# Kernel optimization log

Measured on AMD Instinct MI355X. Metric: run time of the kernel, lower is better.

Reference implementation:

```python
import jax, jax.numpy as jnp
import numpy as np

B = 1048576  # batch size
EPS_CLAMP_LO = 1e-6
EPS_CLAMP_HI = 1.0 - 1e-6


def _build_mask():
    # mask[k, i, j] = 1 iff i + j == k, flattened to [19, 100]
    i = np.arange(10)
    m = np.zeros((19, 10, 10), dtype=np.float32)
    ii, jj = np.meshgrid(i, i, indexing='ij')
    m[(ii + jj).ravel(), ii.ravel(), jj.ravel()] = 1.0
    return jnp.asarray(m.reshape(19, 100))


def setup_inputs() -> dict:
    key = jax.random.key(0)
    k1, k2, k3, k4 = jax.random.split(key, 4)
    # concept probabilities: uniform then normalize rows to sum 1
    p1 = jax.random.uniform(k1, (B, 10), dtype=jnp.float32)
    p1 = p1 / p1.sum(axis=1, keepdims=True)
    p2 = jax.random.uniform(k2, (B, 10), dtype=jnp.float32)
    p2 = p2 / p2.sum(axis=1, keepdims=True)
    # learnable permutation-tree weights (binaryTreeLogicNet leaf maps)
    W1 = jax.random.uniform(k3, (10, 10), dtype=jnp.float32)
    W2 = jax.random.uniform(k4, (10, 10), dtype=jnp.float32)
    mask = _build_mask()
    return {"p1": p1, "p2": p2, "W1": W1, "W2": W2, "mask": mask}


def _minmax_norm(W):
    lo = W.min(axis=1, keepdims=True)
    hi = W.max(axis=1, keepdims=True)
    return (W - lo) / (hi - lo + 1e-8)


def reference(p1, p2, W1, W2, mask):
    # input_to_leaf: learned soft permutation with minmax-normalized weights
    p1p = p1 @ _minmax_norm(W1)                      # [B,10]
    p2p = p2 @ _minmax_norm(W2)                      # [B,10]
    # MinMaxAggregator graded AND at andness=1.0 -> elementwise min over all pairs
    s = jnp.minimum(p1p[:, :, None], p2p[:, None, :])  # [B,10,10]
    one_minus = 1.0 - jnp.clip(s, EPS_CLAMP_LO, EPS_CLAMP_HI)
    log_one_minus = jnp.log(one_minus + 1e-12).reshape(-1, 100)  # [B,100]
    # fused masked reduction over all 19 sum bins: [B,100] @ [100,19]
    log_prod = log_one_minus @ mask.T                # [B,19]
    y_prob = 1.0 - jnp.exp(log_prod)                 # smooth OR per sum class
    y_prob = y_prob / (y_prob.sum(axis=1, keepdims=True) + 1e-9)
    return y_prob
```

## Files before the change

kernel.cpp:

```cpp
#include <hip/hip_runtime.h>


#define NBLOCKS 4096

__global__ __launch_bounds__(256) void bacon_main(
    const float* __restrict__ p1, const float* __restrict__ p2,
    const float* __restrict__ W1, const float* __restrict__ W2,
    float* __restrict__ out)
{
    __shared__ __align__(16) float s_out[4864];
    __shared__ __align__(16) float s_w[240];

    const int t = threadIdx.x;
    const int blk = blockIdx.x;

    float a[10], b[10];
    {
        const float2* g1 = (const float2*)p1 + (size_t)blk * 1280 + t * 5;
        const float2* g2 = (const float2*)p2 + (size_t)blk * 1280 + t * 5;
        #pragma unroll
        for (int e = 0; e < 5; ++e) {
            float2 v1 = g1[e];
            float2 v2 = g2[e];
            a[2 * e] = v1.x; a[2 * e + 1] = v1.y;
            b[2 * e] = v2.x; b[2 * e + 1] = v2.y;
        }
    }

    if (t < 20) {
        const float* row = ((t < 10) ? W1 : W2) + (t % 10) * 10;
        float r[10];
        #pragma unroll
        for (int i = 0; i < 10; ++i) r[i] = row[i];
        float lo = r[0], hi = r[0];
        #pragma unroll
        for (int i = 1; i < 10; ++i) {
            lo = fminf(lo, r[i]);
            hi = fmaxf(hi, r[i]);
        }
        float inv = 1.0f / (hi - lo + 1e-8f);
        float* o = s_w + ((t < 10) ? 0 : 120) + (t % 10) * 12;
        #pragma unroll
        for (int i = 0; i < 10; ++i) o[i] = (r[i] - lo) * inv;
        o[10] = 0.0f; o[11] = 0.0f;
    }
    __syncthreads();

    float A[10], Bv[10];
    #pragma unroll
    for (int i = 0; i < 10; ++i) { A[i] = 1.0f; Bv[i] = 1.0f; }
    #pragma unroll
    for (int k = 0; k < 10; ++k) {
        float ak = a[k], bk = b[k];
        const float4* w1q = (const float4*)(s_w + k * 12);
        const float4* w2q = (const float4*)(s_w + 120 + k * 12);
        float4 u0 = w1q[0], u1 = w1q[1];
        float2 u2 = *(const float2*)(s_w + k * 12 + 8);
        float4 v0 = w2q[0], v1 = w2q[1];
        float2 v2 = *(const float2*)(s_w + 120 + k * 12 + 8);
        A[0] = fmaf(-ak, u0.x, A[0]); A[1] = fmaf(-ak, u0.y, A[1]);
        A[2] = fmaf(-ak, u0.z, A[2]); A[3] = fmaf(-ak, u0.w, A[3]);
        A[4] = fmaf(-ak, u1.x, A[4]); A[5] = fmaf(-ak, u1.y, A[5]);
        A[6] = fmaf(-ak, u1.z, A[6]); A[7] = fmaf(-ak, u1.w, A[7]);
        A[8] = fmaf(-ak, u2.x, A[8]); A[9] = fmaf(-ak, u2.y, A[9]);
        Bv[0] = fmaf(-bk, v0.x, Bv[0]); Bv[1] = fmaf(-bk, v0.y, Bv[1]);
        Bv[2] = fmaf(-bk, v0.z, Bv[2]); Bv[3] = fmaf(-bk, v0.w, Bv[3]);
        Bv[4] = fmaf(-bk, v1.x, Bv[4]); Bv[5] = fmaf(-bk, v1.y, Bv[5]);
        Bv[6] = fmaf(-bk, v1.z, Bv[6]); Bv[7] = fmaf(-bk, v1.w, Bv[7]);
        Bv[8] = fmaf(-bk, v2.x, Bv[8]); Bv[9] = fmaf(-bk, v2.y, Bv[9]);
    }

    float prod[19];
    #pragma unroll
    for (int k = 0; k < 19; ++k) prod[k] = 1.0f;
    #pragma unroll
    for (int i = 0; i < 10; ++i) {
        #pragma unroll
        for (int j = 0; j < 10; ++j) {
            prod[i + j] *= fmaxf(A[i], Bv[j]);
        }
    }

    float y[19];
    float tot = 0.0f;
    #pragma unroll
    for (int k = 0; k < 19; ++k) { y[k] = 1.0f - prod[k]; tot += y[k]; }
    float inv = __builtin_amdgcn_rcpf(tot + 1e-9f);

    #pragma unroll
    for (int k = 0; k < 19; ++k) s_out[t * 19 + k] = y[k] * inv;
    __syncthreads();

    {
        const float4* so = (const float4*)s_out;
        float4* go = (float4*)(out + (size_t)blk * 4864);
        #pragma unroll
        for (int it = 0; it < 5; ++it) {
            int idx = t + it * 256;
            if (idx < 1216) go[idx] = so[idx];
        }
    }
}

extern "C" void kernel_launch(void* const* d_in, const int* in_sizes, int n_in,
                              void* d_out, int out_size, void* d_ws, size_t ws_size,
                              hipStream_t stream) {
    const float* p1 = (const float*)d_in[0];
    const float* p2 = (const float*)d_in[1];
    const float* W1 = (const float*)d_in[2];
    const float* W2 = (const float*)d_in[3];
    bacon_main<<<NBLOCKS, 256, 0, stream>>>(p1, p2, W1, W2, (float*)d_out);
}
```

Measured before the change: 150.5 us.

## Use single-wavefront blocks processing four rows per thread without barriers

The kernel shrinks blocks from 256 threads to one 64-lane wavefront, with each thread handling four batch rows: two tiles of two rows each. This raises per-thread instruction-level parallelism and removes the `__syncthreads` barriers, since the block is a single wave. The aim is to hide memory latency better and to cut barrier and launch overhead per row. The trade-offs are fewer resident waves overall and more register pressure. It also now relies on intra-wave ordering of shared-memory writes and reads with no explicit barrier, including the reuse of `s_out` across the two tiles.

```diff
diff --git a/kernel.cpp b/kernel.cpp
--- a/kernel.cpp
+++ b/kernel.cpp
@@ -3,101 +3,103 @@
 
 #define NBLOCKS 4096
 
-__global__ __launch_bounds__(256) void bacon_main(
+__global__ __launch_bounds__(64, 4) void bacon_main(
     const float* __restrict__ p1, const float* __restrict__ p2,
     const float* __restrict__ W1, const float* __restrict__ W2,
     float* __restrict__ out)
 {
-    __shared__ __align__(16) float s_out[4864];
     __shared__ __align__(16) float s_w[240];
+    __shared__ __align__(16) float s_out[2432];
 
-    const int t = threadIdx.x;
-    const int blk = blockIdx.x;
+    const int l = threadIdx.x;
 
-    float a[10], b[10];
-    {
-        const float2* g1 = (const float2*)p1 + (size_t)blk * 1280 + t * 5;
-        const float2* g2 = (const float2*)p2 + (size_t)blk * 1280 + t * 5;
-        #pragma unroll
-        for (int e = 0; e < 5; ++e) {
-            float2 v1 = g1[e];
-            float2 v2 = g2[e];
-            a[2 * e] = v1.x; a[2 * e + 1] = v1.y;
-            b[2 * e] = v2.x; b[2 * e + 1] = v2.y;
-        }
-    }
-
-    if (t < 20) {
-        const float* row = ((t < 10) ? W1 : W2) + (t % 10) * 10;
+    if (l < 20) {
+        const float* row = ((l < 10) ? W1 : W2) + (l % 10) * 10;
         float r[10];
         #pragma unroll
         for (int i = 0; i < 10; ++i) r[i] = row[i];
         float lo = r[0], hi = r[0];
         #pragma unroll
-        for (int i = 1; i < 10; ++i) {
-            lo = fminf(lo, r[i]);
-            hi = fmaxf(hi, r[i]);
-        }
+        for (int i = 1; i < 10; ++i) { lo = fminf(lo, r[i]); hi = fmaxf(hi, r[i]); }
         float inv = 1.0f / (hi - lo + 1e-8f);
-        float* o = s_w + ((t < 10) ? 0 : 120) + (t % 10) * 12;
+        float* o = s_w + ((l < 10) ? 0 : 120) + (l % 10) * 12;
         #pragma unroll
         for (int i = 0; i < 10; ++i) o[i] = (r[i] - lo) * inv;
         o[10] = 0.0f; o[11] = 0.0f;
     }
-    __syncthreads();
-
-    float A[10], Bv[10];
-    #pragma unroll
-    for (int i = 0; i < 10; ++i) { A[i] = 1.0f; Bv[i] = 1.0f; }
-    #pragma unroll
-    for (int k = 0; k < 10; ++k) {
-        float ak = a[k], bk = b[k];
-        const float4* w1q = (const float4*)(s_w + k * 12);
-        const float4* w2q = (const float4*)(s_w + 120 + k * 12);
-        float4 u0 = w1q[0], u1 = w1q[1];
-        float2 u2 = *(const float2*)(s_w + k * 12 + 8);
-        float4 v0 = w2q[0], v1 = w2q[1];
-        float2 v2 = *(const float2*)(s_w + 120 + k * 12 + 8);
-        A[0] = fmaf(-ak, u0.x, A[0]); A[1] = fmaf(-ak, u0.y, A[1]);
-        A[2] = fmaf(-ak, u0.z, A[2]); A[3] = fmaf(-ak, u0.w, A[3]);
-        A[4] = fmaf(-ak, u1.x, A[4]); A[5] = fmaf(-ak, u1.y, A[5]);
-        A[6] = fmaf(-ak, u1.z, A[6]); A[7] = fmaf(-ak, u1.w, A[7]);
-        A[8] = fmaf(-ak, u2.x, A[8]); A[9] = fmaf(-ak, u2.y, A[9]);
-        Bv[0] = fmaf(-bk, v0.x, Bv[0]); Bv[1] = fmaf(-bk, v0.y, Bv[1]);
-        Bv[2] = fmaf(-bk, v0.z, Bv[2]); Bv[3] = fmaf(-bk, v0.w, Bv[3]);
-        Bv[4] = fmaf(-bk, v1.x, Bv[4]); Bv[5] = fmaf(-bk, v1.y, Bv[5]);
-        Bv[6] = fmaf(-bk, v1.z, Bv[6]); Bv[7] = fmaf(-bk, v1.w, Bv[7]);
-        Bv[8] = fmaf(-bk, v2.x, Bv[8]); Bv[9] = fmaf(-bk, v2.y, Bv[9]);
-    }
-
-    float prod[19];
-    #pragma unroll
-    for (int k = 0; k < 19; ++k) prod[k] = 1.0f;
-    #pragma unroll
-    for (int i = 0; i < 10; ++i) {
-        #pragma unroll
-        for (int j = 0; j < 10; ++j) {
-            prod[i + j] *= fmaxf(A[i], Bv[j]);
-        }
-    }
-
-    float y[19];
-    float tot = 0.0f;
-    #pragma unroll
-    for (int k = 0; k < 19; ++k) { y[k] = 1.0f - prod[k]; tot += y[k]; }
-    float inv = __builtin_amdgcn_rcpf(tot + 1e-9f);
 
     #pragma unroll
-    for (int k = 0; k < 19; ++k) s_out[t * 19 + k] = y[k] * inv;
-    __syncthreads();
+    for (int it = 0; it < 2; ++it) {
+        const size_t tile = (size_t)blockIdx.x * 256 + (size_t)it * 128;
 
-    {
-        const float4* so = (const float4*)s_out;
-        float4* go = (float4*)(out + (size_t)blk * 4864);
+        float a0[10], b0[10], a1[10], b1[10];
+        {
+            const float2* g1 = (const float2*)p1 + (tile + l) * 5;
+            const float2* g2 = (const float2*)p2 + (tile + l) * 5;
+            const float2* h1 = g1 + 64 * 5;
+            const float2* h2 = g2 + 64 * 5;
+            #pragma unroll
+            for (int e = 0; e < 5; ++e) {
+                float2 v;
+                v = g1[e]; a0[2*e] = v.x; a0[2*e+1] = v.y;
+                v = g2[e]; b0[2*e] = v.x; b0[2*e+1] = v.y;
+                v = h1[e]; a1[2*e] = v.x; a1[2*e+1] = v.y;
+                v = h2[e]; b1[2*e] = v.x; b1[2*e+1] = v.y;
+            }
+        }
+
+        float A0[10], B0[10], A1[10], B1[10];
         #pragma unroll
-        for (int it = 0; it < 5; ++it) {
-            int idx = t + it * 256;
-            if (idx < 1216) go[idx] = so[idx];
+        for (int i = 0; i < 10; ++i) { A0[i] = 1.0f; B0[i] = 1.0f; A1[i] = 1.0f; B1[i] = 1.0f; }
+        #pragma unroll
+        for (int k = 0; k < 10; ++k) {
+            float4 u0 = *(const float4*)(s_w + k * 12);
+            float4 u1 = *(const float4*)(s_w + k * 12 + 4);
+            float2 u2 = *(const float2*)(s_w + k * 12 + 8);
+            float4 v0 = *(const float4*)(s_w + 120 + k * 12);
+            float4 v1 = *(const float4*)(s_w + 120 + k * 12 + 4);
+            float2 v2 = *(const float2*)(s_w + 120 + k * 12 + 8);
+            float w1v[10] = {u0.x,u0.y,u0.z,u0.w,u1.x,u1.y,u1.z,u1.w,u2.x,u2.y};
+            float w2v[10] = {v0.x,v0.y,v0.z,v0.w,v1.x,v1.y,v1.z,v1.w,v2.x,v2.y};
+            #pragma unroll
+            for (int i = 0; i < 10; ++i) {
+                A0[i] = fmaf(-a0[k], w1v[i], A0[i]);
+                A1[i] = fmaf(-a1[k], w1v[i], A1[i]);
+                B0[i] = fmaf(-b0[k], w2v[i], B0[i]);
+                B1[i] = fmaf(-b1[k], w2v[i], B1[i]);
+            }
+        }
+
+        float p0[19], p1r[19];
+        #pragma unroll
+        for (int k = 0; k < 19; ++k) { p0[k] = 1.0f; p1r[k] = 1.0f; }
+        #pragma unroll
+        for (int i = 0; i < 10; ++i) {
+            #pragma unroll
+            for (int j = 0; j < 10; ++j) {
+                p0[i + j]  *= fmaxf(A0[i], B0[j]);
+                p1r[i + j] *= fmaxf(A1[i], B1[j]);
+            }
+        }
+
+        float t0 = 0.0f, t1 = 0.0f;
+        #pragma unroll
+        for (int k = 0; k < 19; ++k) { p0[k] = 1.0f - p0[k]; t0 += p0[k];
+                                       p1r[k] = 1.0f - p1r[k]; t1 += p1r[k]; }
+        float i0 = __builtin_amdgcn_rcpf(t0 + 1e-9f);
+        float i1 = __builtin_amdgcn_rcpf(t1 + 1e-9f);
+        #pragma unroll
+        for (int k = 0; k < 19; ++k) {
+            s_out[l * 19 + k]        = p0[k] * i0;
+            s_out[(l + 64) * 19 + k] = p1r[k] * i1;
+        }
+
+        {
+            const float4* so = (const float4*)s_out;
+            float4* go = (float4*)(out + tile * 19);
+            #pragma unroll
+            for (int j = 0; j < 9; ++j) go[l + j * 64] = so[l + j * 64];
+            if (l < 32) go[l + 576] = so[l + 576];
         }
     }
 }
@@ -109,5 +111,5 @@
     const float* p2 = (const float*)d_in[1];
     const float* W1 = (const float*)d_in[2];
     const float* W2 = (const float*)d_in[3];
-    bacon_main<<<NBLOCKS, 256, 0, stream>>>(p1, p2, W1, W2, (float*)d_out);
+    bacon_main<<<NBLOCKS, 64, 0, stream>>>(p1, p2, W1, W2, (float*)d_out);
 }
```

After: 161.2 us. +7.1%, slower.
